# Kernel tuning notes

Hardware: AMD Instinct MI355X
Metric: run time of the kernel (lower is better)

## Reference

```python
import jax, jax.numpy as jnp
import numpy as np

B, T, C_IN = 2, 4096, 1024
INTER, OUT = 1024, 1024
ROPE_DIM = 64
GAMMA = 0.99609375  # 1 - 2**-8
GROUPS = 32
EPS = 1e-6


def setup_inputs() -> dict:
    key = jax.random.key(0)
    k = jax.random.split(key, 4)
    return {
        "X_Q": jax.random.normal(k[0], (B, T, C_IN), dtype=jnp.float32),
        "W_Q": jax.random.normal(k[1], (C_IN, INTER), dtype=jnp.float32) / C_IN,
        "W_K": jax.random.normal(k[2], (C_IN, INTER), dtype=jnp.float32) / C_IN,
        "W_V": jax.random.normal(k[3], (C_IN, OUT), dtype=jnp.float32) / C_IN,
        "gn_weight": jnp.ones((OUT,), dtype=jnp.float32),
        "gn_bias": jnp.zeros((OUT,), dtype=jnp.float32),
    }


def _rope(x):
    # lucidrains RotaryEmbedding: rotate first ROPE_DIM features, pairwise-adjacent
    t = x.shape[-2]
    inv_freq = 1.0 / (10000.0 ** (jnp.arange(0, ROPE_DIM, 2, dtype=jnp.float32) / ROPE_DIM))
    freqs = jnp.arange(t, dtype=jnp.float32)[:, None] * inv_freq[None, :]  # [T, ROPE_DIM/2]
    freqs = jnp.repeat(freqs, 2, axis=-1)                                   # [T, ROPE_DIM]
    cos, sin = jnp.cos(freqs), jnp.sin(freqs)
    xr, xp = x[..., :ROPE_DIM], x[..., ROPE_DIM:]
    x1, x2 = xr[..., 0::2], xr[..., 1::2]
    rot = jnp.stack([-x2, x1], axis=-1).reshape(xr.shape)  # rotate_half (adjacent pairs)
    return jnp.concatenate([xr * cos + rot * sin, xp], axis=-1)


def _group_norm(x, w, b):
    # torch GroupNorm applied on x.reshape(-1, C)
    sh = x.shape
    c = sh[-1]
    xr = x.reshape(-1, GROUPS, c // GROUPS)
    mu = xr.mean(-1, keepdims=True)
    var = xr.var(-1, keepdims=True)
    xn = ((xr - mu) * jax.lax.rsqrt(var + EPS)).reshape(-1, c)
    return (xn * w + b).reshape(sh)


def reference(X_Q, W_Q, W_K, W_V, gn_weight, gn_bias):
    Q = jax.nn.silu(_rope(X_Q @ W_Q))  # [B,T,INTER]
    K = jax.nn.silu(_rope(X_Q @ W_K))
    V = jax.nn.silu(X_Q @ W_V)         # [B,T,OUT]
    A = jnp.einsum('btd,bsd->bts', Q, K)  # [B,T,T]
    # decay mask: original multiplies by _get_D(gamma,T).T -> gamma^(m-n) for m>=n
    n = jnp.arange(T)[:, None]
    m = jnp.arange(T)[None, :]
    upper = m >= n
    Dt = jnp.where(upper, GAMMA ** jnp.where(upper, m - n, 0).astype(jnp.float32), 0.0)
    A = A * Dt
    out = jnp.einsum('bts,bsd->btd', A, V)  # [B,T,OUT]
    # dropout p=0 (eval) -> identity
    return _group_norm(out, gn_weight, gn_bias)
```

## Files before the change

kernel.cpp:

```cpp
#include <hip/hip_runtime.h>


typedef __attribute__((ext_vector_type(8))) short bf16x8;
typedef __attribute__((ext_vector_type(4))) short bf16x4;
typedef __attribute__((ext_vector_type(4))) float f32x4;

#define MFMA16(a, b, c) __builtin_amdgcn_mfma_f32_16x16x32_bf16(a, b, c, 0, 0, 0)

static __device__ __forceinline__ short f2bf(float f) {
  unsigned u = __builtin_bit_cast(unsigned, f);
  u = (u + 0x7fffu + ((u >> 16) & 1u)) >> 16;
  return (short)u;
}

static __device__ __forceinline__ float fast_silu(float v) {
  return v * __builtin_amdgcn_rcpf(1.f + __expf(-v));
}

static __device__ __forceinline__ void gl_lds16(const void* g, void* l) {
  __builtin_amdgcn_global_load_lds(
      (const __attribute__((address_space(1))) void*)g,
      (__attribute__((address_space(3))) void*)l, 16, 0, 0);
}

static __device__ __forceinline__ int swzc(int col, int row) {
  return (((col >> 3) ^ (row & 7)) << 3) | (col & 7);
}

#define T_LEN 4096
#define CIN 1024

#define LOG2G (-0.0056465633f)
#define L2IF (0.41524101f)

__global__ __launch_bounds__(256)
void prep_kernel(const float* __restrict__ X, short* __restrict__ Xb,
                 const float* __restrict__ Wq, const float* __restrict__ Wk,
                 const float* __restrict__ Wv, short* __restrict__ WT) {
  __shared__ short tile[64][72];
  const int bx = blockIdx.x;
  const int tid = threadIdx.x;
  if (bx < 4096) {
    const int gid = bx * 256 + tid;
    const int row = gid >> 7;
    const int c = gid & 127;
    const float* s = &X[(size_t)gid * 8];
    float4 f0 = *(const float4*)s;
    float4 f1 = *(const float4*)(s + 4);
    bf16x8 v = {f2bf(f0.x), f2bf(f0.y), f2bf(f0.z), f2bf(f0.w),
                f2bf(f1.x), f2bf(f1.y), f2bf(f1.z), f2bf(f1.w)};
    const int pc = (c & 0x78) | ((c ^ row) & 7);
    *(bf16x8*)&Xb[(size_t)row * 1024 + pc * 8] = v;
    return;
  }
  const int bx2 = bx - 4096;
  const int k0 = (bx2 & 15) * 64, n0 = ((bx2 >> 4) & 15) * 64, mat = bx2 >> 8;
  const float* __restrict__ W = (mat == 0) ? Wq : (mat == 1) ? Wk : Wv;
  const int r = tid >> 4, c = tid & 15;
#pragma unroll
  for (int i = 0; i < 4; ++i) {
    int row = r + 16 * i;
    float4 f = *(const float4*)&W[(size_t)(k0 + row) * CIN + n0 + c * 4];
    tile[c * 4 + 0][row] = f2bf(f.x);
    tile[c * 4 + 1][row] = f2bf(f.y);
    tile[c * 4 + 2][row] = f2bf(f.z);
    tile[c * 4 + 3][row] = f2bf(f.w);
  }
  __syncthreads();
  const int n = tid >> 2, seg = tid & 3;
  bf16x8 lo = *(const bf16x8*)&tile[n][seg * 16];
  bf16x8 hi = *(const bf16x8*)&tile[n][seg * 16 + 8];
  const int R = mat * 1024 + n0 + n;
  const int a0 = (k0 >> 3) + seg * 2;
  short* base = &WT[(size_t)R * CIN];
  *(bf16x8*)&base[(a0 ^ (n & 7)) * 8] = lo;
  *(bf16x8*)&base[((a0 + 1) ^ (n & 7)) * 8] = hi;
}

#define GEMM_DECLS()                                   \
  const int tid = threadIdx.x;                         \
  const int lane = tid & 63, wave = tid >> 6;          \
  const int wm = wave >> 1, wn = wave & 1;             \
  const int l15 = lane & 15, quad = lane >> 4;         \
  const int srow = tid >> 3;                           \
  const int scol = (tid & 7) * 8;                      \
  const int asw = (l15 & 7);

#define ACC_INIT4(acc)                                 \
  _Pragma("unroll") for (int i = 0; i < 4; ++i)        \
  _Pragma("unroll") for (int j = 0; j < 4; ++j) {      \
    f32x4 z = {0.f, 0.f, 0.f, 0.f};                    \
    acc[i][j] = z;                                     \
  }

#define STAGE_TILE(dst, src, ld, r0, k0, nrows)        \
  _Pragma("unroll") for (int i = 0; i < (nrows) / 32; ++i) \
    gl_lds16(&src[(size_t)((r0) + i * 32 + srow) * (ld) + (k0) + scol], \
             &dst[i * 32 + srow][scol]);

#define FRAG_MFMA44(As, Bs, acc)                                            \
  {                                                                         \
    bf16x8 af[4][2], bfr[4][2];                                             \
    _Pragma("unroll") for (int im = 0; im < 4; ++im)                        \
    _Pragma("unroll") for (int ks = 0; ks < 2; ++ks)                        \
      af[im][ks] = *(const bf16x8*)&As[wm * 64 + im * 16 + l15]             \
                       [((ks * 4 + quad) ^ asw) * 8];                       \
    _Pragma("unroll") for (int in = 0; in < 4; ++in)                        \
    _Pragma("unroll") for (int ks = 0; ks < 2; ++ks)                        \
      bfr[in][ks] = *(const bf16x8*)&Bs[wn * 64 + in * 16 + l15]            \
                        [((ks * 4 + quad) ^ asw) * 8];                      \
    _Pragma("unroll") for (int ks = 0; ks < 2; ++ks)                        \
    _Pragma("unroll") for (int im = 0; im < 4; ++im)                        \
    _Pragma("unroll") for (int in = 0; in < 4; ++in)                        \
      acc[im][in] = MFMA16(af[im][ks], bfr[in][ks], acc[im][in]);           \
  }

__global__ __launch_bounds__(256, 2)
void qkv_gemm(const short* __restrict__ Xb, const short* __restrict__ WT,
              short* __restrict__ Qb, short* __restrict__ Kb,
              short* __restrict__ Vt) {
  __shared__ __align__(16) short As[128][64];
  __shared__ __align__(16) short Bs[128][64];
  GEMM_DECLS();
  const int m0 = blockIdx.x * 128;
  const int c0 = blockIdx.y * 128;

  f32x4 acc[4][4];
  ACC_INIT4(acc);

  for (int k0 = 0; k0 < CIN; k0 += 64) {
    __syncthreads();
    STAGE_TILE(As, Xb, CIN, m0, k0, 128);
    STAGE_TILE(Bs, WT, CIN, c0, k0, 128);
    __syncthreads();
    FRAG_MFMA44(As, Bs, acc);
  }

  const int mat = (c0 >> 10);
  const bool ropeBlk = (mat < 2) && ((c0 & 1023) == 0);
#pragma unroll
  for (int im = 0; im < 4; ++im) {
#pragma unroll
    for (int in = 0; in < 4; ++in) {
      const int c = c0 + wn * 64 + in * 16 + l15;
      const int colm = c & 1023;
      const int mbase = m0 + wm * 64 + im * 16 + quad * 4;
      short vv[4];
      if (ropeBlk && colm < 64) {
        const float invf = exp2f(-L2IF * (float)(colm >> 1));
#pragma unroll
        for (int r = 0; r < 4; ++r) {
          float v = acc[im][in][r];
          int t = (mbase + r) & (T_LEN - 1);
          float partner = __shfl_xor(v, 1, 64);
          float ang = (float)t * invf;
          float s_ = __sinf(ang), c_ = __cosf(ang);
          v = (colm & 1) ? (v * c_ + partner * s_) : (v * c_ - partner * s_);
          vv[r] = f2bf(fast_silu(v));
        }
      } else {
#pragma unroll
        for (int r = 0; r < 4; ++r) vv[r] = f2bf(fast_silu(acc[im][in][r]));
      }
      if (mat == 0) {
#pragma unroll
        for (int r = 0; r < 4; ++r)
          Qb[(size_t)(mbase + r) * 1024 + swzc(colm, mbase + r)] = vv[r];
      } else if (mat == 1) {
#pragma unroll
        for (int r = 0; r < 4; ++r)
          Kb[(size_t)(mbase + r) * 1024 + swzc(colm, mbase + r)] = vv[r];
      } else {
        bf16x4 v4 = {vv[0], vv[1], vv[2], vv[3]};
        *(bf16x4*)&Vt[(size_t)colm * 8192 +
                      (((mbase >> 3) ^ (colm & 7)) << 3) + (mbase & 7)] = v4;
      }
    }
  }
}

__global__ __launch_bounds__(256, 2)
void score_kernel(const short* __restrict__ Qb, const short* __restrict__ Kb,
                  short* __restrict__ Ab) {
  int idx = blockIdx.x;
  int ti = 0;
  while (idx >= 32 - ti) { idx -= 32 - ti; ++ti; }
  const int si = ti + idx;
  const int b = blockIdx.y;
  const int s0 = si * 128, t0 = ti * 128;

  __shared__ __align__(16) short Qs[128][64];
  __shared__ __align__(16) short Ks[128][64];
  GEMM_DECLS();

  f32x4 acc[4][4];
  ACC_INIT4(acc);

  for (int k0 = 0; k0 < 1024; k0 += 64) {
    __syncthreads();
    STAGE_TILE(Qs, Qb, 1024, b * T_LEN + t0, k0, 128);
    STAGE_TILE(Ks, Kb, 1024, b * T_LEN + s0, k0, 128);
    __syncthreads();
    FRAG_MFMA44(Qs, Ks, acc);
  }

#pragma unroll
  for (int im = 0; im < 4; ++im) {
#pragma unroll
    for (int in = 0; in < 4; ++in) {
      int s = s0 + wn * 64 + in * 16 + l15;
#pragma unroll
      for (int r = 0; r < 4; ++r) {
        int t = t0 + wm * 64 + im * 16 + quad * 4 + r;
        int d = s - t;
        float v = acc[im][in][r];
        v = (d < 0) ? 0.f : v * exp2f((float)d * LOG2G);
        Ab[((size_t)(b * T_LEN + t)) * T_LEN + swzc(s, t)] = f2bf(v);
      }
    }
  }
}

__global__ __launch_bounds__(256, 2)
void av_kernel(const short* __restrict__ Ab, const short* __restrict__ Vt,
               const float* __restrict__ gw, const float* __restrict__ gb,
               float* __restrict__ Out) {
  const int p = blockIdx.x, b = blockIdx.y, di = blockIdx.z;
  const int n0 = di * 128;

  __shared__ __align__(16) short As2[2][64][64];
  __shared__ __align__(16) short Vs[2][128][64];
  GEMM_DECLS();

  float w4[4], b4[4];
#pragma unroll
  for (int in = 0; in < 4; ++in) {
    int n = n0 + wn * 64 + in * 16 + l15;
    w4[in] = gw[n];
    b4[in] = gb[n];
  }

#pragma unroll 1
  for (int half = 0; half < 2; ++half) {
    const int ti2 = half ? (63 - p) : p;
    const int t0 = ti2 * 64;
    const int nIt = (T_LEN - t0) >> 6;

    f32x4 acc[2][4];
#pragma unroll
    for (int i = 0; i < 2; ++i)
#pragma unroll
      for (int j = 0; j < 4; ++j) {
        f32x4 z = {0.f, 0.f, 0.f, 0.f};
        acc[i][j] = z;
      }

    STAGE_TILE(As2[0], Ab, T_LEN, b * T_LEN + t0, t0, 64);
    STAGE_TILE(Vs[0], Vt, 8192, n0, b * T_LEN + t0, 128);
    __syncthreads();

#pragma unroll 1
    for (int it = 0; it < nIt; ++it) {
      const int cur = it & 1;
      const int nxt = cur ^ 1;
      if (it + 1 < nIt) {
        const int s = t0 + ((it + 1) << 6);
        STAGE_TILE(As2[nxt], Ab, T_LEN, b * T_LEN + t0, s, 64);
        STAGE_TILE(Vs[nxt], Vt, 8192, n0, b * T_LEN + s, 128);
      }
      bf16x8 af[2][2], bfr[4][2];
#pragma unroll
      for (int im = 0; im < 2; ++im)
#pragma unroll
        for (int ks = 0; ks < 2; ++ks)
          af[im][ks] = *(const bf16x8*)&As2[cur][wm * 32 + im * 16 + l15]
                           [((ks * 4 + quad) ^ asw) * 8];
#pragma unroll
      for (int in = 0; in < 4; ++in)
#pragma unroll
        for (int ks = 0; ks < 2; ++ks)
          bfr[in][ks] = *(const bf16x8*)&Vs[cur][wn * 64 + in * 16 + l15]
                            [((ks * 4 + quad) ^ asw) * 8];
#pragma unroll
      for (int ks = 0; ks < 2; ++ks)
#pragma unroll
        for (int im = 0; im < 2; ++im)
#pragma unroll
          for (int in = 0; in < 4; ++in)
            acc[im][in] = MFMA16(af[im][ks], bfr[in][ks], acc[im][in]);
      __syncthreads();
    }

#pragma unroll
    for (int im = 0; im < 2; ++im) {
#pragma unroll
      for (int r = 0; r < 4; ++r) {
        int t = t0 + wm * 32 + im * 16 + quad * 4 + r;
        float* orow = &Out[((size_t)(b * T_LEN + t)) * 1024];
#pragma unroll
        for (int g = 0; g < 2; ++g) {
          float a0 = acc[im][g * 2][r], a1 = acc[im][g * 2 + 1][r];
          float s = a0 + a1;
          float q = a0 * a0 + a1 * a1;
          s += __shfl_xor(s, 1, 64);
          q += __shfl_xor(q, 1, 64);
          s += __shfl_xor(s, 2, 64);
          q += __shfl_xor(q, 2, 64);
          s += __shfl_xor(s, 4, 64);
          q += __shfl_xor(q, 4, 64);
          s += __shfl_xor(s, 8, 64);
          q += __shfl_xor(q, 8, 64);
          float mean = s * (1.f / 32.f);
          float var = q * (1.f / 32.f) - mean * mean;
          float rstd = rsqrtf(var + 1e-6f);
          int n = n0 + wn * 64 + g * 32 + l15;
          orow[n] = (a0 - mean) * rstd * w4[g * 2] + b4[g * 2];
          orow[n + 16] = (a1 - mean) * rstd * w4[g * 2 + 1] + b4[g * 2 + 1];
        }
      }
    }
  }
}

extern "C" void kernel_launch(void* const* d_in, const int* in_sizes, int n_in,
                              void* d_out, int out_size, void* d_ws,
                              size_t ws_size, hipStream_t stream) {
  const float* X = (const float*)d_in[0];
  const float* Wq = (const float*)d_in[1];
  const float* Wk = (const float*)d_in[2];
  const float* Wv = (const float*)d_in[3];
  const float* gw = (const float*)d_in[4];
  const float* gb = (const float*)d_in[5];
  float* Out = (float*)d_out;

  short* Qb = (short*)d_ws;
  short* Kb = Qb + (size_t)8192 * 1024;
  short* Vt = Kb + (size_t)8192 * 1024;
  short* Ab = Vt + (size_t)8192 * 1024;
  short* Xb = Ab;
  short* WT = Xb + (size_t)8192 * 1024;

  prep_kernel<<<4864, 256, 0, stream>>>(X, Xb, Wq, Wk, Wv, WT);
  qkv_gemm<<<dim3(64, 24), 256, 0, stream>>>(Xb, WT, Qb, Kb, Vt);
  score_kernel<<<dim3(528, 2), 256, 0, stream>>>(Qb, Kb, Ab);
  av_kernel<<<dim3(32, 2, 8), 256, 0, stream>>>(Ab, Vt, gw, gb, Out);
}
```

Baseline: 286.8 us.

## Double-buffer GEMM staging and triple-buffer AV loads with explicit vmcnt waits

The QKV and score GEMMs now use double-buffered LDS tiles, so the next K-slice is prefetched with global-to-LDS loads while MFMAs run on the current one. The AV kernel moves from double to triple buffering with a two-iteration prefetch distance. Both use raw s_barrier plus hand-counted s_waitcnt vmcnt values instead of __syncthreads, aiming to hide load latency behind compute. The cost is twice the LDS per block, which may lower occupancy, and correctness now depends on the hard-coded vmcnt counts matching the number of loads STAGE_TILE issues.

```diff
diff --git a/kernel.cpp b/kernel.cpp
--- a/kernel.cpp
+++ b/kernel.cpp
@@ -119,8 +119,8 @@
 void qkv_gemm(const short* __restrict__ Xb, const short* __restrict__ WT,
               short* __restrict__ Qb, short* __restrict__ Kb,
               short* __restrict__ Vt) {
-  __shared__ __align__(16) short As[128][64];
-  __shared__ __align__(16) short Bs[128][64];
+  __shared__ __align__(16) short As[2][128][64];
+  __shared__ __align__(16) short Bs[2][128][64];
   GEMM_DECLS();
   const int m0 = blockIdx.x * 128;
   const int c0 = blockIdx.y * 128;
@@ -128,12 +128,23 @@
   f32x4 acc[4][4];
   ACC_INIT4(acc);
 
+  STAGE_TILE(As[0], Xb, CIN, m0, 0, 128);
+  STAGE_TILE(Bs[0], WT, CIN, c0, 0, 128);
+  int cur = 0;
+#pragma unroll 1
   for (int k0 = 0; k0 < CIN; k0 += 64) {
-    __syncthreads();
-    STAGE_TILE(As, Xb, CIN, m0, k0, 128);
-    STAGE_TILE(Bs, WT, CIN, c0, k0, 128);
-    __syncthreads();
-    FRAG_MFMA44(As, Bs, acc);
+    __builtin_amdgcn_s_barrier();
+    if (k0 + 64 < CIN) {
+      STAGE_TILE(As[cur ^ 1], Xb, CIN, m0, k0 + 64, 128);
+      STAGE_TILE(Bs[cur ^ 1], WT, CIN, c0, k0 + 64, 128);
+      asm volatile("s_waitcnt vmcnt(8)" ::: "memory");
+    } else {
+      asm volatile("s_waitcnt vmcnt(0)" ::: "memory");
+    }
+    __builtin_amdgcn_s_barrier();
+    __builtin_amdgcn_sched_barrier(0);
+    FRAG_MFMA44(As[cur], Bs[cur], acc);
+    cur ^= 1;
   }
 
   const int mat = (c0 >> 10);
@@ -189,19 +200,30 @@
   const int b = blockIdx.y;
   const int s0 = si * 128, t0 = ti * 128;
 
-  __shared__ __align__(16) short Qs[128][64];
-  __shared__ __align__(16) short Ks[128][64];
+  __shared__ __align__(16) short Qs[2][128][64];
+  __shared__ __align__(16) short Ks[2][128][64];
   GEMM_DECLS();
 
   f32x4 acc[4][4];
   ACC_INIT4(acc);
 
+  STAGE_TILE(Qs[0], Qb, 1024, b * T_LEN + t0, 0, 128);
+  STAGE_TILE(Ks[0], Kb, 1024, b * T_LEN + s0, 0, 128);
+  int cur = 0;
+#pragma unroll 1
   for (int k0 = 0; k0 < 1024; k0 += 64) {
-    __syncthreads();
-    STAGE_TILE(Qs, Qb, 1024, b * T_LEN + t0, k0, 128);
-    STAGE_TILE(Ks, Kb, 1024, b * T_LEN + s0, k0, 128);
-    __syncthreads();
-    FRAG_MFMA44(Qs, Ks, acc);
+    __builtin_amdgcn_s_barrier();
+    if (k0 + 64 < 1024) {
+      STAGE_TILE(Qs[cur ^ 1], Qb, 1024, b * T_LEN + t0, k0 + 64, 128);
+      STAGE_TILE(Ks[cur ^ 1], Kb, 1024, b * T_LEN + s0, k0 + 64, 128);
+      asm volatile("s_waitcnt vmcnt(8)" ::: "memory");
+    } else {
+      asm volatile("s_waitcnt vmcnt(0)" ::: "memory");
+    }
+    __builtin_amdgcn_s_barrier();
+    __builtin_amdgcn_sched_barrier(0);
+    FRAG_MFMA44(Qs[cur], Ks[cur], acc);
+    cur ^= 1;
   }
 
 #pragma unroll
@@ -228,8 +250,8 @@
   const int p = blockIdx.x, b = blockIdx.y, di = blockIdx.z;
   const int n0 = di * 128;
 
-  __shared__ __align__(16) short As2[2][64][64];
-  __shared__ __align__(16) short Vs[2][128][64];
+  __shared__ __align__(16) short As2[3][64][64];
+  __shared__ __align__(16) short Vs[3][128][64];
   GEMM_DECLS();
 
   float w4[4], b4[4];
@@ -255,19 +277,32 @@
         acc[i][j] = z;
       }
 
+    __syncthreads();
     STAGE_TILE(As2[0], Ab, T_LEN, b * T_LEN + t0, t0, 64);
     STAGE_TILE(Vs[0], Vt, 8192, n0, b * T_LEN + t0, 128);
-    __syncthreads();
-
+    if (nIt > 1) {
+      STAGE_TILE(As2[1], Ab, T_LEN, b * T_LEN + t0, t0 + 64, 64);
+      STAGE_TILE(Vs[1], Vt, 8192, n0, b * T_LEN + t0 + 64, 128);
+    }
+
+    int cur = 0;
 #pragma unroll 1
     for (int it = 0; it < nIt; ++it) {
-      const int cur = it & 1;
-      const int nxt = cur ^ 1;
-      if (it + 1 < nIt) {
-        const int s = t0 + ((it + 1) << 6);
-        STAGE_TILE(As2[nxt], Ab, T_LEN, b * T_LEN + t0, s, 64);
-        STAGE_TILE(Vs[nxt], Vt, 8192, n0, b * T_LEN + s, 128);
-      }
+      __builtin_amdgcn_s_barrier();
+      const int nx2 = (cur >= 1) ? cur - 1 : 2;
+      if (it + 2 < nIt) {
+        const int s = t0 + ((it + 2) << 6);
+        STAGE_TILE(As2[nx2], Ab, T_LEN, b * T_LEN + t0, s, 64);
+        STAGE_TILE(Vs[nx2], Vt, 8192, n0, b * T_LEN + s, 128);
+        asm volatile("s_waitcnt vmcnt(12)" ::: "memory");
+      } else if (it + 1 < nIt) {
+        asm volatile("s_waitcnt vmcnt(6)" ::: "memory");
+      } else {
+        asm volatile("s_waitcnt vmcnt(0)" ::: "memory");
+      }
+      __builtin_amdgcn_s_barrier();
+      __builtin_amdgcn_sched_barrier(0);
+
       bf16x8 af[2][2], bfr[4][2];
 #pragma unroll
       for (int im = 0; im < 2; ++im)
@@ -288,7 +323,8 @@
 #pragma unroll
           for (int in = 0; in < 4; ++in)
             acc[im][in] = MFMA16(af[im][ks], bfr[in][ks], acc[im][in]);
-      __syncthreads();
+
+      cur = (cur == 2) ? 0 : cur + 1;
     }
 
 #pragma unroll
```

New measurement: 307.6 us. 7.3% more time.
